# Kernel optimization log

Hardware: AMD Instinct MI355X
Metric: run time of the kernel (lower is better)

Reference implementation:

```python
import jax, jax.numpy as jnp
import numpy as np

B, T1, T2, D, E = 128, 128, 8, 1024, 64


def _router(mh_output, W_route, b_route, W_noise, b_noise, noise_eps, mis_mask):
    # [B, T1, T2, D] -> [B, D]
    pooled = mh_output.mean(axis=(1, 2))
    logits = jax.nn.softmax(pooled @ W_route.T + b_route, axis=-1)          # [B, E]
    noise_raw = pooled @ W_noise.T + b_noise                                # [B, E]
    noise = jax.nn.softmax(noise_eps * jax.nn.softplus(noise_raw), axis=-1)
    noisy = logits + noise                                                  # [B, E]

    n_exp = noisy.shape[-1]
    # full sort via top_k (k = num_experts); per-row variable k handled by masking
    vals, idx = jax.lax.top_k(noisy, n_exp)                                 # [B, E]
    rank = jnp.arange(n_exp)[None, :]
    keep = rank < mis_mask[:, None]                                         # [B, E] bool
    # idx is a permutation of experts per row -> scatter hits each slot once
    rows = jnp.arange(noisy.shape[0])[:, None]
    sparse = jnp.zeros_like(noisy).at[rows, idx].set(jnp.where(keep, vals, 0.0))
    # pad_sequence pads indices with 0 and values with 0.0; the torch scatter_
    # then writes 0.0 into expert 0 for rows where k < num_experts (padded
    padded = mis_mask < n_exp
    sparse = sparse.at[:, 0].set(jnp.where(padded, 0.0, sparse[:, 0]))
    router_output = jax.nn.softmax(sparse, axis=-1)
    return router_output, noisy


def setup_inputs() -> dict:
    key = jax.random.key(0)
    k1, k2, k3, k4, k5, k6, k7 = jax.random.split(key, 7)
    bound = 1.0 / np.sqrt(D)
    return {
        "mh_output": jax.random.normal(k1, (B, T1, T2, D), dtype=jnp.float32),
        "W_route": jax.random.uniform(k2, (E, D), jnp.float32, -bound, bound),
        "b_route": jax.random.uniform(k3, (E,), jnp.float32, -bound, bound),
        "W_noise": jax.random.uniform(k4, (E, D), jnp.float32, -bound, bound),
        "b_noise": jax.random.uniform(k5, (E,), jnp.float32, -bound, bound),
        "noise_eps": jax.random.normal(k6, (B, E), dtype=jnp.float32),
        "mis_mask": jax.random.randint(k7, (B,), 1, E + 1, dtype=jnp.int32),
    }


def reference(mh_output, W_route, b_route, W_noise, b_noise, noise_eps, mis_mask):
    return _router(mh_output, W_route, b_route, W_noise, b_noise, noise_eps, mis_mask)
```

## Files before the change

kernel.cpp:

```cpp
#include <hip/hip_runtime.h>
#include <math.h>

#define BB 128
#define T_TOT 1024
#define DD 1024
#define EE 64
#define SPLIT 32

typedef float vfloat4 __attribute__((ext_vector_type(4)));

__global__ __launch_bounds__(256) void pool_partial(const float* __restrict__ x,
                                                    float* __restrict__ part) {
    const int blk  = blockIdx.x;
    const int b    = blk / SPLIT;
    const int s    = blk % SPLIT;
    const int rows = T_TOT / SPLIT;
    const int tid  = threadIdx.x;

    const vfloat4* p =
        (const vfloat4*)(x + ((size_t)b * T_TOT + (size_t)s * rows) * DD) + tid;
    vfloat4 acc = (vfloat4)(0.f);
#pragma unroll 8
    for (int t = 0; t < rows; ++t) {
        vfloat4 v = __builtin_nontemporal_load(&p[(size_t)t * (DD / 4)]);
        acc += v;
    }
    ((vfloat4*)(part + (size_t)blk * DD))[tid] = acc;
}

__global__ __launch_bounds__(256) void router_kernel(
    const float* __restrict__ part,
    const float* __restrict__ W_route, const float* __restrict__ b_route,
    const float* __restrict__ W_noise, const float* __restrict__ b_noise,
    const float* __restrict__ noise_eps, const int* __restrict__ mis_mask,
    float* __restrict__ out ) {
    __shared__ float s_pooled[DD];
    __shared__ float s_route[EE];
    __shared__ float s_noise[EE];

    const int b   = blockIdx.x;
    const int tid = threadIdx.x;

    {
        vfloat4 acc = (vfloat4)(0.f);
#pragma unroll 8
        for (int s = 0; s < SPLIT; ++s) {
            acc += ((const vfloat4*)(part + (size_t)(b * SPLIT + s) * DD))[tid];
        }
        const float inv = 1.0f / (float)T_TOT;
        ((vfloat4*)s_pooled)[tid] = acc * inv;
    }
    __syncthreads();

    {
        const int wave = tid >> 6;
        const int lane = tid & 63;
        for (int i = 0; i < 16; ++i) {
            const int e = wave * 16 + i;
            const float* wr = W_route + (size_t)e * DD;
            const float* wn = W_noise + (size_t)e * DD;
            float dr = 0.f, dn = 0.f;
#pragma unroll
            for (int j = 0; j < 16; ++j) {
                const float pv = s_pooled[lane + 64 * j];
                dr += pv * wr[lane + 64 * j];
                dn += pv * wn[lane + 64 * j];
            }
            for (int off = 32; off; off >>= 1) {
                dr += __shfl_down(dr, off, 64);
                dn += __shfl_down(dn, off, 64);
            }
            if (lane == 0) {
                s_route[e] = dr + b_route[e];
                s_noise[e] = dn + b_noise[e];
            }
        }
    }
    __syncthreads();

    if (tid < 64) {
        const int e = tid;

        float x = s_route[e];
        float m = x;
        for (int off = 32; off; off >>= 1) m = fmaxf(m, __shfl_xor(m, off, 64));
        float ex = expf(x - m);
        float sum = ex;
        for (int off = 32; off; off >>= 1) sum += __shfl_xor(sum, off, 64);
        const float p_route = ex / sum;

        const float nr = s_noise[e];
        const float sp = fmaxf(nr, 0.f) + log1pf(expf(-fabsf(nr)));
        const float h  = noise_eps[b * EE + e] * sp;
        float m2 = h;
        for (int off = 32; off; off >>= 1) m2 = fmaxf(m2, __shfl_xor(m2, off, 64));
        float ex2 = expf(h - m2);
        float sum2 = ex2;
        for (int off = 32; off; off >>= 1) sum2 += __shfl_xor(sum2, off, 64);
        const float p_noise = ex2 / sum2;

        const float noisy = p_route + p_noise;
        out[(size_t)(BB * EE) + b * EE + e] = noisy;

        const int k = mis_mask[b];
        int cnt = 0;
        for (int j = 0; j < 64; ++j) {
            const float vj = __shfl(noisy, j, 64);
            cnt += (vj > noisy) || (vj == noisy && j < e);
        }
        float sparse = (cnt < k) ? noisy : 0.f;
        if (e == 0 && k < EE) sparse = 0.f;

        float m3 = sparse;
        for (int off = 32; off; off >>= 1) m3 = fmaxf(m3, __shfl_xor(m3, off, 64));
        float ex3 = expf(sparse - m3);
        float sum3 = ex3;
        for (int off = 32; off; off >>= 1) sum3 += __shfl_xor(sum3, off, 64);
        out[b * EE + e] = ex3 / sum3;
    }
}

extern "C" void kernel_launch(void* const* d_in, const int* in_sizes, int n_in,
                              void* d_out, int out_size, void* d_ws, size_t ws_size,
                              hipStream_t stream) {
    const float* mh        = (const float*)d_in[0];
    const float* W_route   = (const float*)d_in[1];
    const float* b_route   = (const float*)d_in[2];
    const float* W_noise   = (const float*)d_in[3];
    const float* b_noise   = (const float*)d_in[4];
    const float* noise_eps = (const float*)d_in[5];
    const int*   mis_mask  = (const int*)d_in[6];
    float* out = (float*)d_out;
    float* ws  = (float*)d_ws;

    pool_partial<<<BB * SPLIT, 256, 0, stream>>>(mh, ws);
    router_kernel<<<BB, 256, 0, stream>>>(ws, W_route, b_route,
                                          W_noise, b_noise, noise_eps, mis_mask, out);
}
```

Measured before the change: 686.0 us.

## Fuse pooling and router into one kernel with last-block-done atomic ticket

Merges the partial-pooling and router kernels into a single launch. Each block pools a slice of rows, writes its partial sum, and bumps a per-batch atomic counter. The last block to finish for a batch reduces the partials and runs the router math. It also halves the split count to 16 (64 rows per block), uses two accumulators for more loads in flight, and adds a memset for the counters. This removes a kernel launch and the gap between the two kernels. In exchange it adds fences, atomics and a memset, and leaves fewer blocks to stream a 512MB input.

```diff
diff --git a/kernel.cpp b/kernel.cpp
--- a/kernel.cpp
+++ b/kernel.cpp
@@ -5,47 +5,56 @@
 #define T_TOT 1024
 #define DD 1024
 #define EE 64
-#define SPLIT 32
+#define SPLIT 16
+#define ROWS (T_TOT / SPLIT)
 
 typedef float vfloat4 __attribute__((ext_vector_type(4)));
 
-__global__ __launch_bounds__(256) void pool_partial(const float* __restrict__ x,
-                                                    float* __restrict__ part) {
-    const int blk  = blockIdx.x;
-    const int b    = blk / SPLIT;
-    const int s    = blk % SPLIT;
-    const int rows = T_TOT / SPLIT;
-    const int tid  = threadIdx.x;
-
-    const vfloat4* p =
-        (const vfloat4*)(x + ((size_t)b * T_TOT + (size_t)s * rows) * DD) + tid;
-    vfloat4 acc = (vfloat4)(0.f);
-#pragma unroll 8
-    for (int t = 0; t < rows; ++t) {
-        vfloat4 v = __builtin_nontemporal_load(&p[(size_t)t * (DD / 4)]);
-        acc += v;
-    }
-    ((vfloat4*)(part + (size_t)blk * DD))[tid] = acc;
-}
-
-__global__ __launch_bounds__(256) void router_kernel(
-    const float* __restrict__ part,
+__global__ __launch_bounds__(256) void fused_router(
+    const float* __restrict__ x,
     const float* __restrict__ W_route, const float* __restrict__ b_route,
     const float* __restrict__ W_noise, const float* __restrict__ b_noise,
     const float* __restrict__ noise_eps, const int* __restrict__ mis_mask,
+    float* __restrict__ part, int* __restrict__ tick,
     float* __restrict__ out ) {
     __shared__ float s_pooled[DD];
     __shared__ float s_route[EE];
     __shared__ float s_noise[EE];
+    __shared__ int   s_last;
 
-    const int b   = blockIdx.x;
+    const int blk = blockIdx.x;
+    const int b   = blk >> 4;
+    const int s   = blk & (SPLIT - 1);
     const int tid = threadIdx.x;
 
     {
+        const vfloat4* p =
+            (const vfloat4*)(x + ((size_t)b * T_TOT + (size_t)s * ROWS) * DD) + tid;
+        vfloat4 a0 = (vfloat4)(0.f);
+        vfloat4 a1 = (vfloat4)(0.f);
+#pragma unroll 8
+        for (int t = 0; t < ROWS / 2; ++t) {
+            a0 += __builtin_nontemporal_load(&p[(size_t)t * (DD / 4)]);
+            a1 += __builtin_nontemporal_load(&p[(size_t)(t + ROWS / 2) * (DD / 4)]);
+        }
+        ((vfloat4*)(part + (size_t)blk * DD))[tid] = a0 + a1;
+    }
+
+    __threadfence();
+    __syncthreads();
+    if (tid == 0) {
+        const int old = atomicAdd(&tick[b], 1);
+        s_last = (old == SPLIT - 1) ? 1 : 0;
+    }
+    __syncthreads();
+    if (!s_last) return;
+    __threadfence();
+
+    {
         vfloat4 acc = (vfloat4)(0.f);
-#pragma unroll 8
-        for (int s = 0; s < SPLIT; ++s) {
-            acc += ((const vfloat4*)(part + (size_t)(b * SPLIT + s) * DD))[tid];
+#pragma unroll
+        for (int q = 0; q < SPLIT; ++q) {
+            acc += ((const vfloat4*)(part + (size_t)(b * SPLIT + q) * DD))[tid];
         }
         const float inv = 1.0f / (float)T_TOT;
         ((vfloat4*)s_pooled)[tid] = acc * inv;
@@ -81,10 +90,10 @@
     if (tid < 64) {
         const int e = tid;
 
-        float x = s_route[e];
-        float m = x;
+        float xv = s_route[e];
+        float m = xv;
         for (int off = 32; off; off >>= 1) m = fmaxf(m, __shfl_xor(m, off, 64));
-        float ex = expf(x - m);
+        float ex = expf(xv - m);
         float sum = ex;
         for (int off = 32; off; off >>= 1) sum += __shfl_xor(sum, off, 64);
         const float p_route = ex / sum;
@@ -130,10 +139,13 @@
     const float* b_noise   = (const float*)d_in[4];
     const float* noise_eps = (const float*)d_in[5];
     const int*   mis_mask  = (const int*)d_in[6];
-    float* out = (float*)d_out;
-    float* ws  = (float*)d_ws;
+    float* out  = (float*)d_out;
+    float* part = (float*)d_ws;
+    int*   tick = (int*)((float*)d_ws + (size_t)BB * SPLIT * DD);
 
-    pool_partial<<<BB * SPLIT, 256, 0, stream>>>(mh, ws);
-    router_kernel<<<BB, 256, 0, stream>>>(ws, W_route, b_route,
-                                          W_noise, b_noise, noise_eps, mis_mask, out);
+    hipMemsetAsync(tick, 0, BB * sizeof(int), stream);
+
+    fused_router<<<BB * SPLIT, 256, 0, stream>>>(mh, W_route, b_route,
+                                                 W_noise, b_noise, noise_eps,
+                                                 mis_mask, part, tick, out);
 }
```

Result: slower. 1.212 ms (+76.6%).
